# Kernel tuning notes

Hardware: AMD Instinct MI355X
Metric: run time of the kernel (lower is better)

Reference implementation:

```python
import jax, jax.numpy as jnp
import numpy as np

# Quantization constants (mirror the torch module's __init__ kwargs)
INPUT_SCALE = 0.0625          # q_in: Quantize(input_scale, 0, qint8)
SCORE_SCALE = 0.00390625      # npu_matmul output_scale for scores (1/256)
PROB_SCALE = 0.00048828125    # q_probs: Quantize(prob_scale, 0, qint8) (1/2048)
I8_MIN, I8_MAX = -128, 127
I16_MIN, I16_MAX = -32768, 32767

D, K, M, N = 256, 256, 256, 65536  # w1:[K,D], x:[D,N], w2:[M,K]


def quantize_i8(x, scale):
    # torch Quantize: round-half-to-even(x/scale) + zp(=0), clamp to int8
    return jnp.clip(jnp.round(x / scale), I8_MIN, I8_MAX).astype(jnp.int8)


def npu_matmul_i16(w_i8, x_i8):
    acc = jnp.matmul(w_i8.astype(jnp.int32), x_i8.astype(jnp.int32))
    return jnp.clip(acc, I16_MIN, I16_MAX).astype(jnp.int16)


def setup_inputs() -> dict:
    key = jax.random.key(0)
    k1, k2, k3 = jax.random.split(key, 3)
    x = jax.random.normal(k1, (D, N), dtype=jnp.float32)
    # weights are pre-quantized int8 values stored as float32 (as in the torch module)
    w1 = jax.random.randint(k2, (K, D), -16, 16).astype(jnp.float32)
    w2 = jax.random.randint(k3, (M, K), -16, 16).astype(jnp.float32)
    return {"x": x, "w1": w1, "w2": w2}


def reference(x, w1, w2):
    x_q = quantize_i8(x, INPUT_SCALE)                       # [D, N] int8
    scores_q = npu_matmul_i16(w1.astype(jnp.int8), x_q)     # [K, N] int16 (quantized, scale=SCORE_SCALE)
    scores = scores_q.astype(jnp.float32) * SCORE_SCALE     # dequantize
    probs = jax.nn.softmax(scores, axis=0)                  # softmax over dim 0
    q_probs = quantize_i8(probs, PROB_SCALE)                # [K, N] int8
    out = npu_matmul_i16(w2.astype(jnp.int8), q_probs)      # [M, N] int16
    return out
```

## Files before the change

kernel.cpp:

```cpp
#include <hip/hip_runtime.h>

typedef int   int4v   __attribute__((ext_vector_type(4)));
typedef float float4v __attribute__((ext_vector_type(4)));

#define N_DIM 65536

__device__ __forceinline__ int quant8(float v) {
    int q = (int)rintf(v);
    q = q > 127 ? 127 : q;
    q = q < -128 ? -128 : q;
    return q;
}

__device__ __forceinline__ int clamp16(int s) {
    s = s > 32767 ? 32767 : s;
    s = s < -32768 ? -32768 : s;
    return s;
}

__device__ __forceinline__ unsigned int qpack(float4v v) {
    int q0 = quant8(v.x * 16.0f);
    int q1 = quant8(v.y * 16.0f);
    int q2 = quant8(v.z * 16.0f);
    int q3 = quant8(v.w * 16.0f);
    return (unsigned int)((q0 & 0xff) | ((q1 & 0xff) << 8) |
                          ((q2 & 0xff) << 16) | ((q3 & 0xff) << 24));
}

__device__ __forceinline__ float fexp2(float a) {
    float r;
    asm("v_exp_f32 %0, %1" : "=v"(r) : "v"(a));
    return r;
}

__global__ __launch_bounds__(256) void quant_weights(const float* __restrict__ w1,
                                                     const float* __restrict__ w2,
                                                     unsigned char* __restrict__ w1q,
                                                     unsigned char* __restrict__ w2q) {
    int idx = blockIdx.x * 256 + threadIdx.x;
    const float* src;
    unsigned char* dst;
    int off;
    if (idx < 16384) { src = w1; dst = w1q; off = idx * 4; }
    else             { src = w2; dst = w2q; off = (idx - 16384) * 4; }
    float4v f = *reinterpret_cast<const float4v*>(src + off);
    unsigned int dw = (unsigned int)(((int)f.x & 0xff) | (((int)f.y & 0xff) << 8) |
                                     (((int)f.z & 0xff) << 16) | (((int)f.w & 0xff) << 24));
    *reinterpret_cast<unsigned int*>(dst + off) = dw;
}

__global__ __launch_bounds__(512, 3) void qdq_main(const float* __restrict__ x,
                                                   const unsigned char* __restrict__ w1q,
                                                   const unsigned char* __restrict__ w2q,
                                                   int* __restrict__ out) {
    __shared__ unsigned char xq[8192];
    __shared__ unsigned char pq[8192];
    __shared__ int   mb[8][32];
    __shared__ float sb[8][32];

    const int tid  = threadIdx.x;
    const int wv   = tid >> 6;
    const int lane = tid & 63;
    const int c    = lane & 15;
    const int g    = lane >> 4;

    const int rsub = lane >> 3;
    const int cg   = lane & 7;
    const int R    = rsub & 3;
    const unsigned int sel1 = (R & 1) ? 0x03070206u : 0x05010400u;
    const unsigned int sel2 = (R & 2) ? 0x07060302u : 0x01000504u;
    const int colsel = (0x3120 >> (R * 4)) & 0xF;
    const int n_t = cg * 4 + colsel;
    const int qb  = rsub & 4;

    int4v a1f[2][4], a2f[2][4];
    {
        const unsigned char* a1 = w1q + (size_t)(wv * 32 + c) * 256 + g * 16;
        const unsigned char* a2 = w2q + (size_t)(wv * 32 + c) * 256 + g * 16;
        #pragma unroll
        for (int rt = 0; rt < 2; ++rt)
            #pragma unroll
            for (int kk = 0; kk < 4; ++kk) {
                a1f[rt][kk] = *reinterpret_cast<const int4v*>(a1 + rt * 4096 + kk * 64);
                a2f[rt][kk] = *reinterpret_cast<const int4v*>(a2 + rt * 4096 + kk * 64);
            }
    }

    const int colstart = blockIdx.x * 256;
    const float* xpb = x + (size_t)(wv * 32 + rsub) * N_DIM + cg * 4;

    float4v raw[4];
    #pragma unroll
    for (int i = 0; i < 4; ++i)
        raw[i] = *reinterpret_cast<const float4v*>(xpb + (size_t)i * (8 * N_DIM) + colstart);

    const float C = 0.0056355275034725134f;

    for (int it = 0; it < 8; ++it) {
        const int col0 = colstart + it * 32;

        unsigned int Wq[4];
        #pragma unroll
        for (int i = 0; i < 4; ++i) Wq[i] = qpack(raw[i]);
        if (it < 7) {
            #pragma unroll
            for (int i = 0; i < 4; ++i)
                raw[i] = *reinterpret_cast<const float4v*>(
                    xpb + (size_t)i * (8 * N_DIM) + (col0 + 32));
        }

        #pragma unroll
        for (int i = 0; i < 4; ++i) {
            unsigned int t = (unsigned int)__shfl_xor((int)Wq[i], 8);
            unsigned int Q = __builtin_amdgcn_perm(t, Wq[i], sel1);
            unsigned int u = (unsigned int)__shfl_xor((int)Q, 16);
            unsigned int F = __builtin_amdgcn_perm(Q, u, sel2);
            const int dbase = wv * 32 + i * 8 + qb;
            *reinterpret_cast<unsigned int*>(
                xq + n_t * 256 + (dbase ^ ((n_t & 15) << 4))) = F;
        }
        __syncthreads();

        int4v bq[2][4];
        #pragma unroll
        for (int t2 = 0; t2 < 2; ++t2)
            #pragma unroll
            for (int kk = 0; kk < 4; ++kk)
                bq[t2][kk] = *reinterpret_cast<const int4v*>(
                    xq + (t2 * 16 + c) * 256 + ((kk * 64 + g * 16) ^ (c << 4)));

        unsigned int scA[4], scB[4];
        int imA = -(1 << 30), imB = -(1 << 30);
        #pragma unroll
        for (int rt = 0; rt < 2; ++rt) {
            int4v accA = {0, 0, 0, 0}, accB = {0, 0, 0, 0};
            #pragma unroll
            for (int kk = 0; kk < 4; ++kk) {
                accA = __builtin_amdgcn_mfma_i32_16x16x64_i8(a1f[rt][kk], bq[0][kk], accA, 0, 0, 0);
                accB = __builtin_amdgcn_mfma_i32_16x16x64_i8(a1f[rt][kk], bq[1][kk], accB, 0, 0, 0);
            }
            {
                const int s0 = clamp16(accA[0]), s1 = clamp16(accA[1]);
                const int s2 = clamp16(accA[2]), s3 = clamp16(accA[3]);
                int m01 = s0 > s1 ? s0 : s1, m23 = s2 > s3 ? s2 : s3;
                int m = m01 > m23 ? m01 : m23;
                imA = imA > m ? imA : m;
                scA[2 * rt]     = (unsigned int)((s0 & 0xffff) | (s1 << 16));
                scA[2 * rt + 1] = (unsigned int)((s2 & 0xffff) | (s3 << 16));
            }
            {
                const int s0 = clamp16(accB[0]), s1 = clamp16(accB[1]);
                const int s2 = clamp16(accB[2]), s3 = clamp16(accB[3]);
                int m01 = s0 > s1 ? s0 : s1, m23 = s2 > s3 ? s2 : s3;
                int m = m01 > m23 ? m01 : m23;
                imB = imB > m ? imB : m;
                scB[2 * rt]     = (unsigned int)((s0 & 0xffff) | (s1 << 16));
                scB[2 * rt + 1] = (unsigned int)((s2 & 0xffff) | (s3 << 16));
            }
        }

        {
            int o = __shfl_xor(imA, 16); imA = imA > o ? imA : o;
            o = __shfl_xor(imA, 32);     imA = imA > o ? imA : o;
            o = __shfl_xor(imB, 16);     imB = imB > o ? imB : o;
            o = __shfl_xor(imB, 32);     imB = imB > o ? imB : o;
        }
        if (g == 0) mb[wv][c] = imA;
        else if (g == 1) mb[wv][16 + c] = imB;
        __syncthreads();
        int gmA = mb[0][c], gmB = mb[0][16 + c];
        #pragma unroll
        for (int j = 1; j < 8; ++j) {
            int a = mb[j][c], b = mb[j][16 + c];
            gmA = gmA > a ? gmA : a;
            gmB = gmB > b ? gmB : b;
        }

        float sA = 0.0f, sB = 0.0f;
        #pragma unroll
        for (int i = 0; i < 4; ++i) {
            sA += fexp2((float)((int)(short)(scA[i] & 0xffffu) - gmA) * C);
            sA += fexp2((float)(((int)scA[i] >> 16) - gmA) * C);
            sB += fexp2((float)((int)(short)(scB[i] & 0xffffu) - gmB) * C);
            sB += fexp2((float)(((int)scB[i] >> 16) - gmB) * C);
        }
        sA += __shfl_xor(sA, 16); sA += __shfl_xor(sA, 32);
        sB += __shfl_xor(sB, 16); sB += __shfl_xor(sB, 32);
        if (g == 0) sb[wv][c] = sA;
        else if (g == 1) sb[wv][16 + c] = sB;
        __syncthreads();
        float gsA = 0.0f, gsB = 0.0f;
        #pragma unroll
        for (int j = 0; j < 8; ++j) { gsA += sb[j][c]; gsB += sb[j][16 + c]; }
        const float qsA = 2048.0f / gsA;
        const float qsB = 2048.0f / gsB;

        #pragma unroll
        for (int rt = 0; rt < 2; ++rt) {
            const int koff = wv * 32 + rt * 16 + g * 4;
            {
                const unsigned int w0 = scA[2 * rt], w1 = scA[2 * rt + 1];
                int q0 = (int)rintf(fexp2((float)((int)(short)(w0 & 0xffffu) - gmA) * C) * qsA);
                int q1 = (int)rintf(fexp2((float)(((int)w0 >> 16) - gmA) * C) * qsA);
                int q2 = (int)rintf(fexp2((float)((int)(short)(w1 & 0xffffu) - gmA) * C) * qsA);
                int q3 = (int)rintf(fexp2((float)(((int)w1 >> 16) - gmA) * C) * qsA);
                q0 = q0 > 127 ? 127 : q0;
                q1 = q1 > 127 ? 127 : q1;
                q2 = q2 > 127 ? 127 : q2;
                q3 = q3 > 127 ? 127 : q3;
                *reinterpret_cast<unsigned int*>(
                    pq + c * 256 + (koff ^ (c << 4))) =
                    (unsigned int)(q0 | (q1 << 8) | (q2 << 16) | (q3 << 24));
            }
            {
                const unsigned int w0 = scB[2 * rt], w1 = scB[2 * rt + 1];
                int q0 = (int)rintf(fexp2((float)((int)(short)(w0 & 0xffffu) - gmB) * C) * qsB);
                int q1 = (int)rintf(fexp2((float)(((int)w0 >> 16) - gmB) * C) * qsB);
                int q2 = (int)rintf(fexp2((float)((int)(short)(w1 & 0xffffu) - gmB) * C) * qsB);
                int q3 = (int)rintf(fexp2((float)(((int)w1 >> 16) - gmB) * C) * qsB);
                q0 = q0 > 127 ? 127 : q0;
                q1 = q1 > 127 ? 127 : q1;
                q2 = q2 > 127 ? 127 : q2;
                q3 = q3 > 127 ? 127 : q3;
                *reinterpret_cast<unsigned int*>(
                    pq + (16 + c) * 256 + (koff ^ (c << 4))) =
                    (unsigned int)(q0 | (q1 << 8) | (q2 << 16) | (q3 << 24));
            }
        }
        __syncthreads();

        int4v b2[2][4];
        #pragma unroll
        for (int t2 = 0; t2 < 2; ++t2)
            #pragma unroll
            for (int kk = 0; kk < 4; ++kk)
                b2[t2][kk] = *reinterpret_cast<const int4v*>(
                    pq + (t2 * 16 + c) * 256 + ((kk * 64 + g * 16) ^ (c << 4)));

        #pragma unroll
        for (int rt = 0; rt < 2; ++rt) {
            int4v accA = {0, 0, 0, 0}, accB = {0, 0, 0, 0};
            #pragma unroll
            for (int kk = 0; kk < 4; ++kk) {
                accA = __builtin_amdgcn_mfma_i32_16x16x64_i8(a2f[rt][kk], b2[0][kk], accA, 0, 0, 0);
                accB = __builtin_amdgcn_mfma_i32_16x16x64_i8(a2f[rt][kk], b2[1][kk], accB, 0, 0, 0);
            }
            #pragma unroll
            for (int r = 0; r < 4; ++r) {
                const size_t rowoff =
                    (size_t)(wv * 32 + rt * 16 + g * 4 + r) * N_DIM + col0;
                out[rowoff + c]      = clamp16(accA[r]);
                out[rowoff + 16 + c] = clamp16(accB[r]);
            }
        }
    }
}

extern "C" void kernel_launch(void* const* d_in, const int* in_sizes, int n_in,
                              void* d_out, int out_size, void* d_ws, size_t ws_size,
                              hipStream_t stream) {
    const float* x  = (const float*)d_in[0];
    const float* w1 = (const float*)d_in[1];
    const float* w2 = (const float*)d_in[2];
    int* out = (int*)d_out;

    unsigned char* w1q = (unsigned char*)d_ws;
    unsigned char* w2q = w1q + 65536;

    quant_weights<<<128, 256, 0, stream>>>(w1, w2, w1q, w2q);
    qdq_main<<<256, 512, 0, stream>>>(x, w1q, w2q, out);
}
```

Before: 42.43 us.

## Fuse softmax max/sum pass, reload w2 fragments per iteration, raise occupancy

Computes the per-wave local max and the local exp-sum before a single barrier, then rescales partial sums by exp2 of the max difference (online-softmax merge). This removes one __syncthreads per column tile. w2 fragments are now reloaded from global memory each iteration instead of kept resident, and the MFMA loops are restructured to one column tile at a time to cut register pressure. Occupancy hint rises from 3 to 4 blocks, and the grid doubles to 512 blocks of 128 columns each. Output stores become nontemporal. The cost is extra exp2 work in the merge and repeated w2 loads, which should mostly hit cache.

```diff
diff --git a/kernel.cpp b/kernel.cpp
--- a/kernel.cpp
+++ b/kernel.cpp
@@ -49,7 +49,7 @@
     *reinterpret_cast<unsigned int*>(dst + off) = dw;
 }
 
-__global__ __launch_bounds__(512, 3) void qdq_main(const float* __restrict__ x,
+__global__ __launch_bounds__(512, 4) void qdq_main(const float* __restrict__ x,
                                                    const unsigned char* __restrict__ w1q,
                                                    const unsigned char* __restrict__ w2q,
                                                    int* __restrict__ out) {
@@ -73,20 +73,18 @@
     const int n_t = cg * 4 + colsel;
     const int qb  = rsub & 4;
 
-    int4v a1f[2][4], a2f[2][4];
+    int4v a1f[2][4];
     {
         const unsigned char* a1 = w1q + (size_t)(wv * 32 + c) * 256 + g * 16;
-        const unsigned char* a2 = w2q + (size_t)(wv * 32 + c) * 256 + g * 16;
         #pragma unroll
         for (int rt = 0; rt < 2; ++rt)
             #pragma unroll
-            for (int kk = 0; kk < 4; ++kk) {
+            for (int kk = 0; kk < 4; ++kk)
                 a1f[rt][kk] = *reinterpret_cast<const int4v*>(a1 + rt * 4096 + kk * 64);
-                a2f[rt][kk] = *reinterpret_cast<const int4v*>(a2 + rt * 4096 + kk * 64);
-            }
     }
-
-    const int colstart = blockIdx.x * 256;
+    const unsigned char* a2 = w2q + (size_t)(wv * 32 + c) * 256 + g * 16;
+
+    const int colstart = blockIdx.x * 128;
     const float* xpb = x + (size_t)(wv * 32 + rsub) * N_DIM + cg * 4;
 
     float4v raw[4];
@@ -96,13 +94,13 @@
 
     const float C = 0.0056355275034725134f;
 
-    for (int it = 0; it < 8; ++it) {
+    for (int it = 0; it < 4; ++it) {
         const int col0 = colstart + it * 32;
 
         unsigned int Wq[4];
         #pragma unroll
         for (int i = 0; i < 4; ++i) Wq[i] = qpack(raw[i]);
-        if (it < 7) {
+        if (it < 3) {
             #pragma unroll
             for (int i = 0; i < 4; ++i)
                 raw[i] = *reinterpret_cast<const float4v*>(
@@ -121,77 +119,75 @@
         }
         __syncthreads();
 
-        int4v bq[2][4];
-        #pragma unroll
-        for (int t2 = 0; t2 < 2; ++t2)
-            #pragma unroll
-            for (int kk = 0; kk < 4; ++kk)
-                bq[t2][kk] = *reinterpret_cast<const int4v*>(
+        unsigned int sc[2][4];
+        int im[2];
+        #pragma unroll
+        for (int t2 = 0; t2 < 2; ++t2) {
+            int4v bq[4];
+            #pragma unroll
+            for (int kk = 0; kk < 4; ++kk)
+                bq[kk] = *reinterpret_cast<const int4v*>(
                     xq + (t2 * 16 + c) * 256 + ((kk * 64 + g * 16) ^ (c << 4)));
-
-        unsigned int scA[4], scB[4];
-        int imA = -(1 << 30), imB = -(1 << 30);
-        #pragma unroll
-        for (int rt = 0; rt < 2; ++rt) {
-            int4v accA = {0, 0, 0, 0}, accB = {0, 0, 0, 0};
-            #pragma unroll
-            for (int kk = 0; kk < 4; ++kk) {
-                accA = __builtin_amdgcn_mfma_i32_16x16x64_i8(a1f[rt][kk], bq[0][kk], accA, 0, 0, 0);
-                accB = __builtin_amdgcn_mfma_i32_16x16x64_i8(a1f[rt][kk], bq[1][kk], accB, 0, 0, 0);
-            }
-            {
-                const int s0 = clamp16(accA[0]), s1 = clamp16(accA[1]);
-                const int s2 = clamp16(accA[2]), s3 = clamp16(accA[3]);
+            int imt = -(1 << 30);
+            #pragma unroll
+            for (int rt = 0; rt < 2; ++rt) {
+                int4v acc = {0, 0, 0, 0};
+                #pragma unroll
+                for (int kk = 0; kk < 4; ++kk)
+                    acc = __builtin_amdgcn_mfma_i32_16x16x64_i8(a1f[rt][kk], bq[kk], acc, 0, 0, 0);
+                const int s0 = clamp16(acc[0]), s1 = clamp16(acc[1]);
+                const int s2 = clamp16(acc[2]), s3 = clamp16(acc[3]);
                 int m01 = s0 > s1 ? s0 : s1, m23 = s2 > s3 ? s2 : s3;
                 int m = m01 > m23 ? m01 : m23;
-                imA = imA > m ? imA : m;
-                scA[2 * rt]     = (unsigned int)((s0 & 0xffff) | (s1 << 16));
-                scA[2 * rt + 1] = (unsigned int)((s2 & 0xffff) | (s3 << 16));
-            }
-            {
-                const int s0 = clamp16(accB[0]), s1 = clamp16(accB[1]);
-                const int s2 = clamp16(accB[2]), s3 = clamp16(accB[3]);
-                int m01 = s0 > s1 ? s0 : s1, m23 = s2 > s3 ? s2 : s3;
-                int m = m01 > m23 ? m01 : m23;
-                imB = imB > m ? imB : m;
-                scB[2 * rt]     = (unsigned int)((s0 & 0xffff) | (s1 << 16));
-                scB[2 * rt + 1] = (unsigned int)((s2 & 0xffff) | (s3 << 16));
-            }
-        }
+                imt = imt > m ? imt : m;
+                sc[t2][2 * rt]     = (unsigned int)((s0 & 0xffff) | (s1 << 16));
+                sc[t2][2 * rt + 1] = (unsigned int)((s2 & 0xffff) | (s3 << 16));
+            }
+            im[t2] = imt;
+        }
+
+        int4v a2f[2][4];
+        #pragma unroll
+        for (int rt = 0; rt < 2; ++rt)
+            #pragma unroll
+            for (int kk = 0; kk < 4; ++kk)
+                a2f[rt][kk] = *reinterpret_cast<const int4v*>(a2 + rt * 4096 + kk * 64);
 
         {
-            int o = __shfl_xor(imA, 16); imA = imA > o ? imA : o;
-            o = __shfl_xor(imA, 32);     imA = imA > o ? imA : o;
-            o = __shfl_xor(imB, 16);     imB = imB > o ? imB : o;
-            o = __shfl_xor(imB, 32);     imB = imB > o ? imB : o;
-        }
-        if (g == 0) mb[wv][c] = imA;
-        else if (g == 1) mb[wv][16 + c] = imB;
+            int o = __shfl_xor(im[0], 16); im[0] = im[0] > o ? im[0] : o;
+            o = __shfl_xor(im[0], 32);     im[0] = im[0] > o ? im[0] : o;
+            o = __shfl_xor(im[1], 16);     im[1] = im[1] > o ? im[1] : o;
+            o = __shfl_xor(im[1], 32);     im[1] = im[1] > o ? im[1] : o;
+        }
+        if (g == 0) mb[wv][c] = im[0];
+        else if (g == 1) mb[wv][16 + c] = im[1];
+        float s0 = 0.0f, s1 = 0.0f;
+        #pragma unroll
+        for (int i = 0; i < 4; ++i) {
+            s0 += fexp2((float)((int)(short)(sc[0][i] & 0xffffu) - im[0]) * C);
+            s0 += fexp2((float)(((int)sc[0][i] >> 16) - im[0]) * C);
+            s1 += fexp2((float)((int)(short)(sc[1][i] & 0xffffu) - im[1]) * C);
+            s1 += fexp2((float)(((int)sc[1][i] >> 16) - im[1]) * C);
+        }
+        s0 += __shfl_xor(s0, 16); s0 += __shfl_xor(s0, 32);
+        s1 += __shfl_xor(s1, 16); s1 += __shfl_xor(s1, 32);
+        if (g == 0) sb[wv][c] = s0;
+        else if (g == 1) sb[wv][16 + c] = s1;
         __syncthreads();
-        int gmA = mb[0][c], gmB = mb[0][16 + c];
-        #pragma unroll
-        for (int j = 1; j < 8; ++j) {
+
+        int gmA = -(1 << 30), gmB = -(1 << 30);
+        #pragma unroll
+        for (int j = 0; j < 8; ++j) {
             int a = mb[j][c], b = mb[j][16 + c];
             gmA = gmA > a ? gmA : a;
             gmB = gmB > b ? gmB : b;
         }
-
-        float sA = 0.0f, sB = 0.0f;
-        #pragma unroll
-        for (int i = 0; i < 4; ++i) {
-            sA += fexp2((float)((int)(short)(scA[i] & 0xffffu) - gmA) * C);
-            sA += fexp2((float)(((int)scA[i] >> 16) - gmA) * C);
-            sB += fexp2((float)((int)(short)(scB[i] & 0xffffu) - gmB) * C);
-            sB += fexp2((float)(((int)scB[i] >> 16) - gmB) * C);
-        }
-        sA += __shfl_xor(sA, 16); sA += __shfl_xor(sA, 32);
-        sB += __shfl_xor(sB, 16); sB += __shfl_xor(sB, 32);
-        if (g == 0) sb[wv][c] = sA;
-        else if (g == 1) sb[wv][16 + c] = sB;
-        __syncthreads();
         float gsA = 0.0f, gsB = 0.0f;
         #pragma unroll
-        for (int j = 0; j < 8; ++j) { gsA += sb[j][c]; gsB += sb[j][16 + c]; }
+        for (int j = 0; j < 8; ++j) {
+            gsA += sb[j][c]      * fexp2((float)(mb[j][c] - gmA) * C);
+            gsB += sb[j][16 + c] * fexp2((float)(mb[j][16 + c] - gmB) * C);
+        }
         const float qsA = 2048.0f / gsA;
         const float qsB = 2048.0f / gsB;
 
@@ -199,7 +195,7 @@
         for (int rt = 0; rt < 2; ++rt) {
             const int koff = wv * 32 + rt * 16 + g * 4;
             {
-                const unsigned int w0 = scA[2 * rt], w1 = scA[2 * rt + 1];
+                const unsigned int w0 = sc[0][2 * rt], w1 = sc[0][2 * rt + 1];
                 int q0 = (int)rintf(fexp2((float)((int)(short)(w0 & 0xffffu) - gmA) * C) * qsA);
                 int q1 = (int)rintf(fexp2((float)(((int)w0 >> 16) - gmA) * C) * qsA);
                 int q2 = (int)rintf(fexp2((float)((int)(short)(w1 & 0xffffu) - gmA) * C) * qsA);
@@ -213,7 +209,7 @@
                     (unsigned int)(q0 | (q1 << 8) | (q2 << 16) | (q3 << 24));
             }
             {
-                const unsigned int w0 = scB[2 * rt], w1 = scB[2 * rt + 1];
+                const unsigned int w0 = sc[1][2 * rt], w1 = sc[1][2 * rt + 1];
                 int q0 = (int)rintf(fexp2((float)((int)(short)(w0 & 0xffffu) - gmB) * C) * qsB);
                 int q1 = (int)rintf(fexp2((float)(((int)w0 >> 16) - gmB) * C) * qsB);
                 int q2 = (int)rintf(fexp2((float)((int)(short)(w1 & 0xffffu) - gmB) * C) * qsB);
@@ -229,28 +225,26 @@
         }
         __syncthreads();
 
-        int4v b2[2][4];
-        #pragma unroll
-        for (int t2 = 0; t2 < 2; ++t2)
-            #pragma unroll
-            for (int kk = 0; kk < 4; ++kk)
-                b2[t2][kk] = *reinterpret_cast<const int4v*>(
+        #pragma unroll
+        for (int t2 = 0; t2 < 2; ++t2) {
+            int4v b2[4];
+            #pragma unroll
+            for (int kk = 0; kk < 4; ++kk)
+                b2[kk] = *reinterpret_cast<const int4v*>(
                     pq + (t2 * 16 + c) * 256 + ((kk * 64 + g * 16) ^ (c << 4)));
-
-        #pragma unroll
-        for (int rt = 0; rt < 2; ++rt) {
-            int4v accA = {0, 0, 0, 0}, accB = {0, 0, 0, 0};
-            #pragma unroll
-            for (int kk = 0; kk < 4; ++kk) {
-                accA = __builtin_amdgcn_mfma_i32_16x16x64_i8(a2f[rt][kk], b2[0][kk], accA, 0, 0, 0);
-                accB = __builtin_amdgcn_mfma_i32_16x16x64_i8(a2f[rt][kk], b2[1][kk], accB, 0, 0, 0);
-            }
-            #pragma unroll
-            for (int r = 0; r < 4; ++r) {
-                const size_t rowoff =
-                    (size_t)(wv * 32 + rt * 16 + g * 4 + r) * N_DIM + col0;
-                out[rowoff + c]      = clamp16(accA[r]);
-                out[rowoff + 16 + c] = clamp16(accB[r]);
+            #pragma unroll
+            for (int rt = 0; rt < 2; ++rt) {
+                int4v acc = {0, 0, 0, 0};
+                #pragma unroll
+                for (int kk = 0; kk < 4; ++kk)
+                    acc = __builtin_amdgcn_mfma_i32_16x16x64_i8(a2f[rt][kk], b2[kk], acc, 0, 0, 0);
+                #pragma unroll
+                for (int r = 0; r < 4; ++r) {
+                    const size_t rowoff =
+                        (size_t)(wv * 32 + rt * 16 + g * 4 + r) * N_DIM + col0;
+                    __builtin_nontemporal_store(clamp16(acc[r]),
+                                                &out[rowoff + t2 * 16 + c]);
+                }
             }
         }
     }
@@ -268,5 +262,5 @@
     unsigned char* w2q = w1q + 65536;
 
     quant_weights<<<128, 256, 0, stream>>>(w1, w2, w1q, w2q);
-    qdq_main<<<256, 512, 0, stream>>>(x, w1q, w2q, out);
-}
+    qdq_main<<<512, 512, 0, stream>>>(x, w1q, w2q, out);
+}
```

New measurement: 83.46 us. +96.7%, slower.
